# Kernel optimization log

Measured on AMD Instinct MI355X. Metric: run time of the kernel, lower is better.

The kernel has to match this reference:

```python
import jax, jax.numpy as jnp
import numpy as np
import math

B, S, D, H = 2, 2048, 1024, 16
DH = D // H

def setup_inputs() -> dict:
    key0 = jax.random.key(0)
    ks = jax.random.split(key0, 12)
    s = 1.0 / math.sqrt(D)
    return {
        "query": jax.random.normal(ks[0], (B, S, D), jnp.float32),
        "key": jax.random.normal(ks[1], (B, S, D), jnp.float32),
        "value": jax.random.normal(ks[2], (B, S, D), jnp.float32),
        "mask": jax.random.randint(ks[3], (B, 1, S, S), 0, 2, jnp.int32),
        "Wq": jax.random.normal(ks[4], (D, D), jnp.float32) * s,
        "bq": jnp.zeros((D,), jnp.float32),
        "Wk": jax.random.normal(ks[5], (D, D), jnp.float32) * s,
        "bk": jnp.zeros((D,), jnp.float32),
        "Wv": jax.random.normal(ks[6], (D, D), jnp.float32) * s,
        "bv": jnp.zeros((D,), jnp.float32),
        "Wo": jax.random.normal(ks[7], (D, D), jnp.float32) * s,
        "bo": jnp.zeros((D,), jnp.float32),
    }

def reference(query, key, value, mask, Wq, bq, Wk, bk, Wv, bv, Wo, bo):
    # Linear projections (torch Linear: x @ W.T + b)
    q = query @ Wq.T + bq
    k = key @ Wk.T + bk
    v = value @ Wv.T + bv
    # [B, S, D] -> [B, H, S, DH]
    q = q.reshape(B, S, H, DH).transpose(0, 2, 1, 3)
    k = k.reshape(B, S, H, DH).transpose(0, 2, 1, 3)
    v = v.reshape(B, S, H, DH).transpose(0, 2, 1, 3)
    # scaled dot-product attention with explicit [B,H,S,S] scores
    score = jnp.einsum('bhqd,bhkd->bhqk', q, k) / math.sqrt(DH)
    score = jnp.where(mask == 0, jnp.float32(-1e9), score)
    attn = jax.nn.softmax(score, axis=-1)
    out = jnp.einsum('bhqk,bhkd->bhqd', attn, v)
    out = out.transpose(0, 2, 1, 3).reshape(B, S, D)
    return out @ Wo.T + bo
```

## Files before the change

kernel.cpp:

```cpp
#include <hip/hip_runtime.h>
#include <hip/hip_bf16.h>

typedef __attribute__((ext_vector_type(4))) float f32x4;
typedef __attribute__((ext_vector_type(8))) short bf16x8;
typedef __attribute__((ext_vector_type(4))) short s16x4;
typedef __attribute__((ext_vector_type(4))) unsigned int u32x4;
typedef unsigned short ushort_t;
typedef unsigned int u32;
typedef unsigned long long u64;

constexpr int B = 2, S = 2048, D = 1024, H = 16, DH = 64;

__device__ __forceinline__ ushort_t f2bf(float f) {
    union { float f; unsigned int i; } v; v.f = f;
    unsigned int r = v.i + 0x7fffu + ((v.i >> 16) & 1u);
    return (ushort_t)(r >> 16);
}

__device__ __forceinline__ float fast_exp2(float x) {
#if __has_builtin(__builtin_amdgcn_exp2f)
    return __builtin_amdgcn_exp2f(x);
#else
    return exp2f(x);
#endif
}

__device__ __forceinline__ void gload_lds16(const void* g, void* l) {
    __builtin_amdgcn_global_load_lds(
        (const __attribute__((address_space(1))) unsigned int*)g,
        (__attribute__((address_space(3))) unsigned int*)l,
        16, 0, 0);
}

__global__ __launch_bounds__(256) void cvt_f32_bf16(
    const float* __restrict__ in, ushort_t* __restrict__ out, int n)
{
    int i = (blockIdx.x * 256 + threadIdx.x) * 4;
    if (i >= n) return;
    f32x4 v = *(const f32x4*)(in + i);
    s16x4 o;
    for (int j = 0; j < 4; ++j) o[j] = (short)f2bf(v[j]);
    *(s16x4*)(out + i) = o;
}

__global__ __launch_bounds__(256) void cvt3_f32_bf16(
    const float* __restrict__ a0, const float* __restrict__ a1,
    const float* __restrict__ a2, ushort_t* __restrict__ out, int n)
{
    const float* in = blockIdx.y == 0 ? a0 : (blockIdx.y == 1 ? a1 : a2);
    int i = (blockIdx.x * 256 + threadIdx.x) * 4;
    if (i >= n) return;
    f32x4 v = *(const f32x4*)(in + i);
    s16x4 o;
    for (int j = 0; j < 4; ++j) o[j] = (short)f2bf(v[j]);
    *(s16x4*)(out + (size_t)blockIdx.y * n + i) = o;
}

__global__ __launch_bounds__(256) void cvt4_f32_bf16(
    const float* __restrict__ a0, const float* __restrict__ a1,
    const float* __restrict__ a2, const float* __restrict__ a3,
    ushort_t* __restrict__ out, int n)
{
    const float* in = blockIdx.y == 0 ? a0 : (blockIdx.y == 1 ? a1 :
                      (blockIdx.y == 2 ? a2 : a3));
    int i = (blockIdx.x * 256 + threadIdx.x) * 4;
    if (i >= n) return;
    f32x4 v = *(const f32x4*)(in + i);
    s16x4 o;
    for (int j = 0; j < 4; ++j) o[j] = (short)f2bf(v[j]);
    *(s16x4*)(out + (size_t)blockIdx.y * n + i) = o;
}

__global__ __launch_bounds__(256) void pack_mask(
    const int* __restrict__ mask, u64* __restrict__ pm)
{
    const int wave_g = (blockIdx.x * 256 + threadIdx.x) >> 6;
    const int lane = threadIdx.x & 63;
    for (int w = 0; w < 16; ++w) {
        size_t idx = (size_t)wave_g * 16 + w;
        int mv = mask[idx * 64 + lane];
        u64 bal = __ballot(mv != 0);
        if (lane == 0) {
            int t = (int)(idx & 31);
            int q = (int)((idx >> 5) & (S - 1));
            int b = (int)(idx >> 16);
            pm[((size_t)b * 32 + t) * S + q] = bal;
        }
    }
}

__global__ __launch_bounds__(256) void transpose_v(
    const ushort_t* __restrict__ Vw, ushort_t* __restrict__ Vt)
{
    __shared__ ushort_t T[64][80];
    const int st = blockIdx.x, bh = blockIdx.y;
    const int b = bh / H, h = bh % H;
    const int tid = threadIdx.x;
    const int r = tid >> 3, c = tid & 7;
    for (int p = 0; p < 2; ++p) {
        int s = p * 32 + r;
        bf16x8 v = *(const bf16x8*)(Vw + (size_t)(b * S + st * 64 + s) * D + h * DH + c * 8);
        *(bf16x8*)(&T[s][c * 8]) = v;
    }
    __syncthreads();
    const int q0q = (c >> 2) * 8 + (c & 3);
    for (int p = 0; p < 2; ++p) {
        int d = p * 32 + r;
        bf16x8 o;
        for (int j = 0; j < 4; ++j) o[j]     = (short)T[q0q * 4 + j][d];
        for (int j = 0; j < 4; ++j) o[4 + j] = (short)T[(q0q + 4) * 4 + j][d];
        *(bf16x8*)(Vt + (size_t)((b * H + h) * DH + d) * S + st * 64 + c * 8) = o;
    }
}

template <typename OutT>
__device__ __forceinline__ void gemm_body(
    const ushort_t* __restrict__ Ag,
    const ushort_t* __restrict__ Wg,
    const float* __restrict__ bias,
    OutT* __restrict__ Cg,
    int M, int N, int K,
    ushort_t* As, ushort_t* Bs)
{
    constexpr int BK = 64;
    const int tid  = threadIdx.x;
    const int wid  = tid >> 6;
    const int lane = tid & 63;
    const int m0 = blockIdx.x * 128;
    const int n0 = blockIdx.y * 128;
    const int wr = wid >> 1, wc = wid & 1;

    const int lrow = lane & 15;
    const int lk8  = (lane >> 4) * 8;
    const int srow  = lane >> 3;
    const int sbyte = (lane & 7) * 16;

    f32x4 acc[4][4] = {};

    for (int k0 = 0; k0 < K; k0 += BK) {
        for (int c = 0; c < 4; ++c) {
            int r0 = wid * 32 + c * 8;
            gload_lds16((const char*)(Ag + (size_t)(m0 + r0 + srow) * K + k0) + sbyte,
                        (char*)As + r0 * 128);
            gload_lds16((const char*)(Wg + (size_t)(n0 + r0 + srow) * K + k0) + sbyte,
                        (char*)Bs + r0 * 128);
        }
        __syncthreads();

        for (int kk = 0; kk < BK; kk += 32) {
            bf16x8 af[4], bfr[4];
            for (int i = 0; i < 4; ++i) {
                af[i]  = *(const bf16x8*)(As + (wr * 64 + i * 16 + lrow) * BK + kk + lk8);
                bfr[i] = *(const bf16x8*)(Bs + (wc * 64 + i * 16 + lrow) * BK + kk + lk8);
            }
            for (int i = 0; i < 4; ++i)
                for (int j = 0; j < 4; ++j)
                    acc[i][j] = __builtin_amdgcn_mfma_f32_16x16x32_bf16(
                        af[i], bfr[j], acc[i][j], 0, 0, 0);
        }
        __syncthreads();
    }

    const int crow0 = (lane >> 4) * 4;
    const int ccol  = lane & 15;
    for (int j = 0; j < 4; ++j) {
        int col = n0 + wc * 64 + j * 16 + ccol;
        float bv = bias[col];
        for (int i = 0; i < 4; ++i) {
            for (int r = 0; r < 4; ++r) {
                int row = m0 + wr * 64 + i * 16 + crow0 + r;
                float val = acc[i][j][r] + bv;
                if constexpr (__is_same(OutT, float))
                    Cg[(size_t)row * N + col] = val;
                else
                    Cg[(size_t)row * N + col] = f2bf(val);
            }
        }
    }
}

template <typename OutT>
__global__ __launch_bounds__(256, 2) void gemm_bt_bias(
    const ushort_t* __restrict__ Ag, const ushort_t* __restrict__ Wg,
    const float* __restrict__ bias, OutT* __restrict__ Cg,
    int M, int N, int K)
{
    __shared__ ushort_t As[128 * 64];
    __shared__ ushort_t Bs[128 * 64];
    gemm_body<OutT>(Ag, Wg, bias, Cg, M, N, K, As, Bs);
}

__global__ __launch_bounds__(256, 2) void gemm_qkv(
    const ushort_t* __restrict__ X3,
    const ushort_t* __restrict__ W4,
    const float* __restrict__ b0, const float* __restrict__ b1,
    const float* __restrict__ b2,
    ushort_t* __restrict__ QKV,
    int M, int N, int K)
{
    __shared__ ushort_t As[128 * 64];
    __shared__ ushort_t Bs[128 * 64];
    const int z = blockIdx.z;
    const float* bias = z == 0 ? b0 : (z == 1 ? b1 : b2);
    gemm_body<ushort_t>(X3 + (size_t)z * M * K, W4 + (size_t)z * N * K,
                        bias, QKV + (size_t)z * M * N, M, N, K, As, Bs);
}

__global__ __launch_bounds__(256, 4) void attn_kernel(
    const ushort_t* __restrict__ Q,
    const ushort_t* __restrict__ Kt,
    const ushort_t* __restrict__ Vt,
    const u64* __restrict__ pmask,
    ushort_t* __restrict__ O)
{
    constexpr int KVBLK = 64;
    constexpr float C1 = 0.18033688f;
    constexpr float C2 = 17.31234049f;
    __shared__ ushort_t Ks[KVBLK * DH];
    __shared__ ushort_t Vs[DH * KVBLK];

    const int tid  = threadIdx.x;
    const int wid  = tid >> 6;
    const int lane = tid & 63;
    const int qt = blockIdx.x;
    const int bh = blockIdx.y;
    const int b = bh / H, h = bh % H;
    const int q0 = qt * 64 + wid * 16;

    const int lq   = lane & 15;
    const int hi   = lane >> 4;
    const int lk8  = hi * 8;
    const int srow = lane >> 3;
    const int sbyte = (((lane & 7) ^ srow) & 7) * 16;

    bf16x8 qf[2];
    for (int kk = 0; kk < 2; ++kk)
        qf[kk] = *(const bf16x8*)(Q + (size_t)(b * S + q0 + lq) * D + h * DH + kk * 32 + lk8);

    f32x4 oacc[4] = {};
    float psum = 0.f;

    const u64* pmrow = pmask + (size_t)b * 32 * S + q0 + lq;
    const ushort_t* Vtb = Vt + (size_t)(b * H + h) * DH * S;

    for (int kv0 = 0; kv0 < S; kv0 += KVBLK) {
        for (int c = 0; c < 2; ++c) {
            int r0 = wid * 16 + c * 8;
            gload_lds16((const char*)(Kt + (size_t)(b * S + kv0 + r0 + srow) * D + h * DH) + sbyte,
                        (char*)Ks + r0 * 128);
            gload_lds16((const char*)(Vtb + (size_t)(r0 + srow) * S + kv0) + sbyte,
                        (char*)Vs + r0 * 128);
        }
        const u64 mw = pmrow[(size_t)(kv0 >> 6) * S];
        __syncthreads();

        f32x4 sc[4] = {};
        for (int kk = 0; kk < 2; ++kk) {
            for (int ni = 0; ni < 4; ++ni) {
                int kchunk = ((kk * 4 + hi) ^ (lq & 7)) * 8;
                bf16x8 kf = *(const bf16x8*)(Ks + (ni * 16 + lq) * 64 + kchunk);
                sc[ni] = __builtin_amdgcn_mfma_f32_16x16x32_bf16(kf, qf[kk], sc[ni], 0, 0, 0);
            }
        }

        const u64 sh = mw >> (hi * 4);
        const u32 lo32 = (u32)sh;
        const u32 hi32 = (u32)(sh >> 32);
        u32 paw[8];
        #pragma unroll
        for (int ni = 0; ni < 4; ++ni) {
            u32 word = (ni < 2) ? lo32 : hi32;
            const int base = (ni & 1) * 16;
            u32 pw[4];
            #pragma unroll
            for (int r = 0; r < 4; ++r) {
                float x = __builtin_fmaf(sc[ni][r], C1, -C2);
                float p = fast_exp2(x);
                int mbit = ((int)(word << (31 - (base + r)))) >> 31;
                u32 pb = __builtin_bit_cast(u32, p) & (u32)mbit & 0xffff0000u;
                psum += __builtin_bit_cast(float, pb);
                pw[r] = pb;
            }
            paw[ni * 2]     = pw[1] | (pw[0] >> 16);
            paw[ni * 2 + 1] = pw[3] | (pw[2] >> 16);
        }

        #pragma unroll
        for (int kk = 0; kk < 2; ++kk) {
            u32x4 pv = {paw[kk * 4], paw[kk * 4 + 1], paw[kk * 4 + 2], paw[kk * 4 + 3]};
            bf16x8 paf = __builtin_bit_cast(bf16x8, pv);
            #pragma unroll
            for (int di = 0; di < 4; ++di) {
                int vchunk = ((kk * 4 + hi) ^ (lq & 7)) * 8;
                bf16x8 vf = *(const bf16x8*)(Vs + (di * 16 + lq) * 64 + vchunk);
                oacc[di] = __builtin_amdgcn_mfma_f32_16x16x32_bf16(paf, vf, oacc[di], 0, 0, 0);
            }
        }
        __syncthreads();
    }

    psum += __shfl_xor(psum, 16, 64);
    psum += __shfl_xor(psum, 32, 64);
    float inv[4];
    #pragma unroll
    for (int r = 0; r < 4; ++r) {
        int srcb = (hi * 4 + r) << 2;
        float ls = __builtin_bit_cast(float,
            __builtin_amdgcn_ds_bpermute(srcb, __builtin_bit_cast(int, psum)));
        inv[r] = 1.0f / ls;
    }

    #pragma unroll
    for (int di = 0; di < 4; ++di) {
        #pragma unroll
        for (int r = 0; r < 4; ++r) {
            float v = oacc[di][r] * inv[r];
            O[(size_t)(b * S + q0 + hi * 4 + r) * D + h * DH + di * 16 + lq] = f2bf(v);
        }
    }
}

extern "C" void kernel_launch(void* const* d_in, const int* in_sizes, int n_in,
                              void* d_out, int out_size, void* d_ws, size_t ws_size,
                              hipStream_t stream) {
    const float* query = (const float*)d_in[0];
    const float* key   = (const float*)d_in[1];
    const float* value = (const float*)d_in[2];
    const int*   mask  = (const int*)d_in[3];
    const float* Wq = (const float*)d_in[4];
    const float* bq = (const float*)d_in[5];
    const float* Wk = (const float*)d_in[6];
    const float* bk = (const float*)d_in[7];
    const float* Wv = (const float*)d_in[8];
    const float* bv = (const float*)d_in[9];
    const float* Wo = (const float*)d_in[10];
    const float* bo = (const float*)d_in[11];
    float* out = (float*)d_out;

    const int M = B * S;
    const int NX = M * D;
    const int NW = D * D;

    char* ws = (char*)d_ws;
    const size_t MB = 1024 * 1024;
    dim3 gblk(M / 128, D / 128);
    const int gcX = NX / (4 * 256);
    const int gcW = NW / (4 * 256);
    const int pmBlocks = (B * S * (S / 64)) / (16 * 4);

    if (ws_size >= 58 * MB) {
        ushort_t* X3  = (ushort_t*)(ws);
        ushort_t* Vtb = (ushort_t*)(ws);
        ushort_t* Ow  = (ushort_t*)(ws + 8 * MB);
        ushort_t* W4  = (ushort_t*)(ws + 24 * MB);
        ushort_t* QKV = (ushort_t*)(ws + 32 * MB);
        ushort_t* Qw = QKV, *Kw = QKV + NX, *Vw = QKV + 2 * (size_t)NX;
        u64* pm = (u64*)(ws + 56 * MB);

        cvt3_f32_bf16<<<dim3(gcX, 3), 256, 0, stream>>>(query, key, value, X3, NX);
        cvt4_f32_bf16<<<dim3(gcW, 4), 256, 0, stream>>>(Wq, Wk, Wv, Wo, W4, NW);
        pack_mask<<<pmBlocks, 256, 0, stream>>>(mask, pm);

        gemm_qkv<<<dim3(M / 128, D / 128, 3), 256, 0, stream>>>(
            X3, W4, bq, bk, bv, QKV, M, D, D);

        transpose_v<<<dim3(S / 64, B * H), 256, 0, stream>>>(Vw, Vtb);
        attn_kernel<<<dim3(S / 64, B * H), 256, 0, stream>>>(Qw, Kw, Vtb, pm, Ow);

        gemm_bt_bias<float><<<gblk, 256, 0, stream>>>(Ow, W4 + 3 * (size_t)NW, bo, out, M, D, D);
    } else {
        ushort_t* Xb = (ushort_t*)(ws);
        ushort_t* Vtb = (ushort_t*)(ws);
        ushort_t* Wb = (ushort_t*)(ws + 8  * MB);
        u64*      pm = (u64*)(ws + 8 * MB);
        ushort_t* Qw = (ushort_t*)(ws + 16 * MB);
        ushort_t* Kw = (ushort_t*)(ws + 24 * MB);
        ushort_t* Vw = (ushort_t*)(ws + 32 * MB);
        ushort_t* Ow = (ushort_t*)(ws + 40 * MB);

        cvt_f32_bf16<<<gcX, 256, 0, stream>>>(query, Xb, NX);
        cvt_f32_bf16<<<gcW, 256, 0, stream>>>(Wq, Wb, NW);
        gemm_bt_bias<ushort_t><<<gblk, 256, 0, stream>>>(Xb, Wb, bq, Qw, M, D, D);

        cvt_f32_bf16<<<gcX, 256, 0, stream>>>(key, Xb, NX);
        cvt_f32_bf16<<<gcW, 256, 0, stream>>>(Wk, Wb, NW);
        gemm_bt_bias<ushort_t><<<gblk, 256, 0, stream>>>(Xb, Wb, bk, Kw, M, D, D);

        cvt_f32_bf16<<<gcX, 256, 0, stream>>>(value, Xb, NX);
        cvt_f32_bf16<<<gcW, 256, 0, stream>>>(Wv, Wb, NW);
        gemm_bt_bias<ushort_t><<<gblk, 256, 0, stream>>>(Xb, Wb, bv, Vw, M, D, D);

        transpose_v<<<dim3(S / 64, B * H), 256, 0, stream>>>(Vw, Vtb);
        pack_mask<<<pmBlocks, 256, 0, stream>>>(mask, pm);

        attn_kernel<<<dim3(S / 64, B * H), 256, 0, stream>>>(Qw, Kw, Vtb, pm, Ow);

        cvt_f32_bf16<<<gcW, 256, 0, stream>>>(Wo, Wb, NW);
        gemm_bt_bias<float><<<gblk, 256, 0, stream>>>(Ow, Wb, bo, out, M, D, D);
    }
}
```

Baseline: 152.1 us.

## Double-buffer K/V LDS tiles in attention to overlap loads with MFMA

The attention kernel now keeps two LDS buffers for K and V. The next KV tile and its mask word are prefetched while the current tile is computed, and there is one wait-plus-barrier per iteration instead of a load, sync, compute, sync sequence. This is meant to hide global-to-LDS latency behind the QK and PV MFMAs. It doubles LDS use per block, which may reduce occupancy under the 4-blocks launch bound.

```diff
diff --git a/kernel.cpp b/kernel.cpp
--- a/kernel.cpp
+++ b/kernel.cpp
@@ -214,10 +214,11 @@
     ushort_t* __restrict__ O)
 {
     constexpr int KVBLK = 64;
+    constexpr int NT = S / KVBLK;
     constexpr float C1 = 0.18033688f;
     constexpr float C2 = 17.31234049f;
-    __shared__ ushort_t Ks[KVBLK * DH];
-    __shared__ ushort_t Vs[DH * KVBLK];
+    __shared__ ushort_t Ks[2][KVBLK * DH];
+    __shared__ ushort_t Vs[2][KVBLK * DH];
 
     const int tid  = threadIdx.x;
     const int wid  = tid >> 6;
@@ -243,27 +244,48 @@
     const u64* pmrow = pmask + (size_t)b * 32 * S + q0 + lq;
     const ushort_t* Vtb = Vt + (size_t)(b * H + h) * DH * S;
 
-    for (int kv0 = 0; kv0 < S; kv0 += KVBLK) {
+    {
         for (int c = 0; c < 2; ++c) {
             int r0 = wid * 16 + c * 8;
-            gload_lds16((const char*)(Kt + (size_t)(b * S + kv0 + r0 + srow) * D + h * DH) + sbyte,
-                        (char*)Ks + r0 * 128);
-            gload_lds16((const char*)(Vtb + (size_t)(r0 + srow) * S + kv0) + sbyte,
-                        (char*)Vs + r0 * 128);
-        }
-        const u64 mw = pmrow[(size_t)(kv0 >> 6) * S];
-        __syncthreads();
-
+            gload_lds16((const char*)(Kt + (size_t)(b * S + r0 + srow) * D + h * DH) + sbyte,
+                        (char*)Ks[0] + r0 * 128);
+            gload_lds16((const char*)(Vtb + (size_t)(r0 + srow) * S) + sbyte,
+                        (char*)Vs[0] + r0 * 128);
+        }
+    }
+    u64 mwcur = pmrow[0];
+    asm volatile("s_waitcnt vmcnt(0)" ::: "memory");
+    __builtin_amdgcn_s_barrier();
+
+    int cur = 0;
+    for (int t = 0; t < NT; ++t) {
+        u64 mwnxt = 0;
+        if (t + 1 < NT) {
+            const int kvn = (t + 1) * KVBLK;
+            for (int c = 0; c < 2; ++c) {
+                int r0 = wid * 16 + c * 8;
+                gload_lds16((const char*)(Kt + (size_t)(b * S + kvn + r0 + srow) * D + h * DH) + sbyte,
+                            (char*)Ks[cur ^ 1] + r0 * 128);
+                gload_lds16((const char*)(Vtb + (size_t)(r0 + srow) * S + kvn) + sbyte,
+                            (char*)Vs[cur ^ 1] + r0 * 128);
+            }
+            mwnxt = pmrow[(size_t)(t + 1) * S];
+        }
+
+        const ushort_t* Kc = Ks[cur];
+        const ushort_t* Vc = Vs[cur];
         f32x4 sc[4] = {};
+        #pragma unroll
         for (int kk = 0; kk < 2; ++kk) {
+            const int chunk = ((kk * 4 + hi) ^ (lq & 7)) * 8;
+            #pragma unroll
             for (int ni = 0; ni < 4; ++ni) {
-                int kchunk = ((kk * 4 + hi) ^ (lq & 7)) * 8;
-                bf16x8 kf = *(const bf16x8*)(Ks + (ni * 16 + lq) * 64 + kchunk);
+                bf16x8 kf = *(const bf16x8*)(Kc + (ni * 16 + lq) * 64 + chunk);
                 sc[ni] = __builtin_amdgcn_mfma_f32_16x16x32_bf16(kf, qf[kk], sc[ni], 0, 0, 0);
             }
         }
 
-        const u64 sh = mw >> (hi * 4);
+        const u64 sh = mwcur >> (hi * 4);
         const u32 lo32 = (u32)sh;
         const u32 hi32 = (u32)(sh >> 32);
         u32 paw[8];
@@ -289,14 +311,18 @@
         for (int kk = 0; kk < 2; ++kk) {
             u32x4 pv = {paw[kk * 4], paw[kk * 4 + 1], paw[kk * 4 + 2], paw[kk * 4 + 3]};
             bf16x8 paf = __builtin_bit_cast(bf16x8, pv);
+            const int chunk = ((kk * 4 + hi) ^ (lq & 7)) * 8;
             #pragma unroll
             for (int di = 0; di < 4; ++di) {
-                int vchunk = ((kk * 4 + hi) ^ (lq & 7)) * 8;
-                bf16x8 vf = *(const bf16x8*)(Vs + (di * 16 + lq) * 64 + vchunk);
+                bf16x8 vf = *(const bf16x8*)(Vc + (di * 16 + lq) * 64 + chunk);
                 oacc[di] = __builtin_amdgcn_mfma_f32_16x16x32_bf16(paf, vf, oacc[di], 0, 0, 0);
             }
         }
-        __syncthreads();
+
+        asm volatile("s_waitcnt vmcnt(0)" ::: "memory");
+        __builtin_amdgcn_s_barrier();
+        cur ^= 1;
+        mwcur = mwnxt;
     }
 
     psum += __shfl_xor(psum, 16, 64);
```

After: 154.0 us. About the same (+1.2%).
